# Optimization experiments

Measured on AMD Instinct MI355X. Metric: run time of the kernel, lower is better.

The kernel has to match this reference:

```python
import jax, jax.numpy as jnp
import numpy as np
import math

B, S, E, H = 4, 1024, 768, 12
HD = E // H

def setup_inputs() -> dict:
    key = jax.random.key(0)
    ks = jax.random.split(key, 13)
    inp = {
        'query': jax.random.normal(ks[0], (B, S, E), jnp.float32),
        'key':   jax.random.normal(ks[1], (B, S, E), jnp.float32),
        'value': jax.random.normal(ks[2], (B, S, E), jnp.float32),
        'mask':  jax.random.randint(ks[3], (B, S, S), 0, 2, jnp.int32),
    }
    scale = 1.0 / math.sqrt(E)
    for i, nm in enumerate(['q', 'k', 'v', 'o']):
        inp[f'W{nm}'] = jax.random.normal(ks[4 + 2 * i], (E, E), jnp.float32) * scale
        inp[f'b{nm}'] = jax.random.normal(ks[5 + 2 * i], (E,), jnp.float32) * 0.01
    return inp


def reference(query, key, value, mask, Wq, bq, Wk, bk, Wv, bv, Wo, bo):
    # QKV projections (torch Linear: x @ W.T + b), split into heads -> [B,H,S,HD]
    def proj(x, W, b):
        y = x @ W.T + b
        return y.reshape(B, S, H, HD).transpose(0, 2, 1, 3)

    q = proj(query, Wq, bq)
    k = proj(key, Wk, bk)
    v = proj(value, Wv, bv)

    scores = jnp.einsum('bhqd,bhkd->bhqk', q, k) / jnp.sqrt(jnp.float32(HD))
    m = mask[:, None, :, :]  # [B,1,S,S] broadcast over heads
    # multiply-then-masked_fill semantics of the original module
    scores = scores * m.astype(scores.dtype)
    scores = jnp.where(m == 0, -jnp.inf, scores)
    attn = jax.nn.softmax(scores, axis=-1)
    # nan_to_num for fully-masked rows (all -inf -> NaN -> 0)
    attn = jnp.where(jnp.isnan(attn), 0.0, attn)
    # dropout omitted (eval/deterministic reference)
    xv = jnp.einsum('bhqk,bhkd->bhqd', attn, v)
    xv = xv.transpose(0, 2, 1, 3).reshape(B, S, E)
    out = xv @ Wo.T + bo
    return out
```

## Files before the change

### kernel.cpp

```cpp
#include <hip/hip_runtime.h>

typedef __bf16 bf16x8 __attribute__((ext_vector_type(8)));
typedef float floatx4 __attribute__((ext_vector_type(4)));

#define B_ 4
#define S_ 1024
#define E_ 768
#define H_ 12
#define HD_ 64

__device__ __forceinline__ void async16(const void* g, void* l) {
  __builtin_amdgcn_global_load_lds((const __attribute__((address_space(1))) void*)g,
                                   (__attribute__((address_space(3))) void*)l, 16, 0, 0);
}

__device__ __forceinline__ floatx4 mfma16(bf16x8 a, bf16x8 b, floatx4 c) {
  return __builtin_amdgcn_mfma_f32_16x16x32_bf16(a, b, c, 0, 0, 0);
}

__global__ __launch_bounds__(256) void prep_kernel(
    const float* __restrict__ q, const float* __restrict__ k, const float* __restrict__ v,
    const float* __restrict__ w0, const float* __restrict__ w1,
    const float* __restrict__ w2, const float* __restrict__ w3,
    const int* __restrict__ mask,
    __bf16* __restrict__ xin, __bf16* __restrict__ wb,
    unsigned long long* __restrict__ bm) {
  const int bx = blockIdx.x;
  if (bx < 4608) {
    const int z = bx / 1536, xb = bx % 1536;
    const float* s = (z == 0) ? q : (z == 1) ? k : v;
    __bf16* d = xin + (size_t)z * (size_t)(B_ * S_ * E_);
    const size_t i8 = (size_t)xb * 256 + threadIdx.x;
    const float4* sp = (const float4*)s + i8 * 2;
    float4 a = sp[0], bb = sp[1];
    bf16x8 o;
    o[0] = (__bf16)a.x; o[1] = (__bf16)a.y; o[2] = (__bf16)a.z; o[3] = (__bf16)a.w;
    o[4] = (__bf16)bb.x; o[5] = (__bf16)bb.y; o[6] = (__bf16)bb.z; o[7] = (__bf16)bb.w;
    *(bf16x8*)(d + i8 * 8) = o;
  } else if (bx < 5760) {
    const int t = bx - 4608;
    const int z = t / 288, xb = t % 288;
    const float* s = (z == 0) ? w0 : (z == 1) ? w1 : (z == 2) ? w2 : w3;
    __bf16* d = wb + (size_t)z * (size_t)(E_ * E_);
    const size_t i8 = (size_t)xb * 256 + threadIdx.x;
    const float4* sp = (const float4*)s + i8 * 2;
    float4 a = sp[0], bb = sp[1];
    bf16x8 o;
    o[0] = (__bf16)a.x; o[1] = (__bf16)a.y; o[2] = (__bf16)a.z; o[3] = (__bf16)a.w;
    o[4] = (__bf16)bb.x; o[5] = (__bf16)bb.y; o[6] = (__bf16)bb.z; o[7] = (__bf16)bb.w;
    *(bf16x8*)(d + i8 * 8) = o;
  } else {
    const int row = bx - 5760;
    const int wave = threadIdx.x >> 6, lane = threadIdx.x & 63;
#pragma unroll
    for (int pass = 0; pass < 4; ++pass) {
      const int kk = pass * 256 + wave * 64 + lane;
      const int mv = mask[(size_t)row * S_ + kk];
      const unsigned long long bal = __ballot(mv != 0);
      if (lane == 0) bm[(size_t)row * 16 + pass * 4 + wave] = bal;
    }
  }
}

__global__ __launch_bounds__(256, 2) void proj_qkv_kernel(
    const __bf16* __restrict__ Xq, const __bf16* __restrict__ Xk, const __bf16* __restrict__ Xv,
    const __bf16* __restrict__ Wq, const __bf16* __restrict__ Wk, const __bf16* __restrict__ Wv,
    const float* __restrict__ bq, const float* __restrict__ bk, const float* __restrict__ bv,
    __bf16* __restrict__ Qf, __bf16* __restrict__ Kf, __bf16* __restrict__ Vt) {
  const int z = blockIdx.z;
  const __bf16* X = (z == 0) ? Xq : (z == 1) ? Xk : Xv;
  const __bf16* W = (z == 0) ? Wq : (z == 1) ? Wk : Wv;
  const float* bias = (z == 0) ? bq : (z == 1) ? bk : bv;

  const int tid = threadIdx.x;
  const int wave = tid >> 6, lane = tid & 63;
  const int l15 = lane & 15, quad = lane >> 4;
  const int wr = wave >> 1, wc = wave & 1;
  const int bm = blockIdx.x * 128, bn = blockIdx.y * 128;
  const int srl = lane >> 3, sch = lane & 7;

  __shared__ alignas(16) unsigned char smem[65536];
  __bf16* ST = (__bf16*)smem + (size_t)wave * (64 * 72);

  floatx4 zf = {0.0f, 0.0f, 0.0f, 0.0f};
  floatx4 acc[4][4];
#pragma unroll
  for (int i = 0; i < 4; ++i)
#pragma unroll
    for (int j = 0; j < 4; ++j) acc[i][j] = zf;

#pragma unroll
  for (int c = 0; c < 4; ++c) {
    const int s = c * 4 + wave;
    const int row = s * 8 + srl;
    const int xo = (sch ^ (row & 7)) * 8;
    async16(X + (size_t)(bm + row) * E_ + xo, (__bf16*)smem + s * 512);
    async16(W + (size_t)(bn + row) * E_ + xo, (__bf16*)(smem + 16384) + s * 512);
  }

  for (int kt = 0; kt < 12; ++kt) {
    const int p = kt & 1;
    __bf16* As = (__bf16*)(smem + p * 32768);
    __bf16* Bs = (__bf16*)(smem + p * 32768 + 16384);
    __syncthreads();

    if (kt < 11) {
      const int kk = (kt + 1) * 64;
      __bf16* An = (__bf16*)(smem + (1 - p) * 32768);
      __bf16* Bn = (__bf16*)(smem + (1 - p) * 32768 + 16384);
#pragma unroll
      for (int c = 0; c < 4; ++c) {
        const int s = c * 4 + wave;
        const int row = s * 8 + srl;
        const int xo = (sch ^ (row & 7)) * 8;
        async16(X + (size_t)(bm + row) * E_ + kk + xo, An + s * 512);
        async16(W + (size_t)(bn + row) * E_ + kk + xo, Bn + s * 512);
      }
    }

#pragma unroll
    for (int ks = 0; ks < 2; ++ks) {
      bf16x8 af[4], bfr[4];
#pragma unroll
      for (int i = 0; i < 4; ++i) {
        const int m = wr * 64 + i * 16 + l15;
        af[i] = *(const bf16x8*)&As[m * 64 + (((ks * 4 + quad) ^ (m & 7)) * 8)];
      }
#pragma unroll
      for (int j = 0; j < 4; ++j) {
        const int n = wc * 64 + j * 16 + l15;
        bfr[j] = *(const bf16x8*)&Bs[n * 64 + (((ks * 4 + quad) ^ (n & 7)) * 8)];
      }
#pragma unroll
      for (int i = 0; i < 4; ++i)
#pragma unroll
        for (int j = 0; j < 4; ++j)
          acc[i][j] = mfma16(af[i], bfr[j], acc[i][j]);
    }
  }
  __syncthreads();

  if (z < 2) {
    __bf16* dst = (z == 0) ? Qf : Kf;
    const float sc = (z == 0) ? 0.125f : 1.0f;
#pragma unroll
    for (int j = 0; j < 4; ++j) {
      const float bval = bias[bn + wc * 64 + j * 16 + l15];
#pragma unroll
      for (int i = 0; i < 4; ++i)
#pragma unroll
        for (int r = 0; r < 4; ++r)
          ST[(i * 16 + quad * 4 + r) * 72 + j * 16 + l15] =
              (__bf16)((acc[i][j][r] + bval) * sc);
    }
#pragma unroll
    for (int t = 0; t < 8; ++t) {
      const int row = t * 8 + (lane >> 3), ch = lane & 7;
      bf16x8 vrow = *(const bf16x8*)&ST[row * 72 + ch * 8];
      *(bf16x8*)&dst[(size_t)(bm + wr * 64 + row) * E_ + bn + wc * 64 + ch * 8] = vrow;
    }
  } else {
#pragma unroll
    for (int j = 0; j < 4; ++j) {
      const float bval = bias[bn + wc * 64 + j * 16 + l15];
#pragma unroll
      for (int i = 0; i < 4; ++i)
#pragma unroll
        for (int r = 0; r < 4; ++r)
          ST[(j * 16 + l15) * 72 + i * 16 + quad * 4 + r] = (__bf16)(acc[i][j][r] + bval);
    }
    const int hh = (bn + wc * 64) >> 6;
    const int m0 = bm + wr * 64;
    const int bb = m0 >> 10, ss0 = m0 & 1023;
#pragma unroll
    for (int t = 0; t < 8; ++t) {
      const int d = t * 8 + (lane >> 3), ch = lane & 7;
      bf16x8 vrow = *(const bf16x8*)&ST[d * 72 + ch * 8];
      *(bf16x8*)&Vt[(((size_t)bb * H_ + hh) * HD_ + d) * S_ + ss0 + ch * 8] = vrow;
    }
  }
}

__global__ __launch_bounds__(256, 4) void proj_out_kernel(
    const __bf16* __restrict__ X, const __bf16* __restrict__ W,
    const float* __restrict__ bias, float* __restrict__ out) {
  const int tid = threadIdx.x;
  const int wave = tid >> 6, lane = tid & 63;
  const int l15 = lane & 15, quad = lane >> 4;
  const int wr = wave >> 1, wc = wave & 1;
  const int bm = blockIdx.x * 64, bn = blockIdx.y * 64;
  const int srl = lane >> 3, sch = lane & 7;

  __shared__ alignas(16) unsigned char smem[32768];

  floatx4 zf = {0.0f, 0.0f, 0.0f, 0.0f};
  floatx4 acc[2][2];
#pragma unroll
  for (int i = 0; i < 2; ++i)
#pragma unroll
    for (int j = 0; j < 2; ++j) acc[i][j] = zf;

#pragma unroll
  for (int c = 0; c < 2; ++c) {
    const int s = c * 4 + wave;
    const int row = s * 8 + srl;
    const int xo = (sch ^ (row & 7)) * 8;
    async16(X + (size_t)(bm + row) * E_ + xo, (__bf16*)smem + s * 512);
    async16(W + (size_t)(bn + row) * E_ + xo, (__bf16*)(smem + 8192) + s * 512);
  }

  for (int kt = 0; kt < 12; ++kt) {
    const int p = kt & 1;
    __bf16* As = (__bf16*)(smem + p * 16384);
    __bf16* Bs = (__bf16*)(smem + p * 16384 + 8192);
    __syncthreads();

    if (kt < 11) {
      const int kk = (kt + 1) * 64;
      __bf16* An = (__bf16*)(smem + (1 - p) * 16384);
      __bf16* Bn = (__bf16*)(smem + (1 - p) * 16384 + 8192);
#pragma unroll
      for (int c = 0; c < 2; ++c) {
        const int s = c * 4 + wave;
        const int row = s * 8 + srl;
        const int xo = (sch ^ (row & 7)) * 8;
        async16(X + (size_t)(bm + row) * E_ + kk + xo, An + s * 512);
        async16(W + (size_t)(bn + row) * E_ + kk + xo, Bn + s * 512);
      }
    }

#pragma unroll
    for (int ks = 0; ks < 2; ++ks) {
      bf16x8 af[2], bfr[2];
#pragma unroll
      for (int i = 0; i < 2; ++i) {
        const int m = wr * 32 + i * 16 + l15;
        af[i] = *(const bf16x8*)&As[m * 64 + (((ks * 4 + quad) ^ (m & 7)) * 8)];
      }
#pragma unroll
      for (int j = 0; j < 2; ++j) {
        const int n = wc * 32 + j * 16 + l15;
        bfr[j] = *(const bf16x8*)&Bs[n * 64 + (((ks * 4 + quad) ^ (n & 7)) * 8)];
      }
#pragma unroll
      for (int i = 0; i < 2; ++i)
#pragma unroll
        for (int j = 0; j < 2; ++j)
          acc[i][j] = mfma16(af[i], bfr[j], acc[i][j]);
    }
  }

#pragma unroll
  for (int j = 0; j < 2; ++j) {
    const int n = bn + wc * 32 + j * 16 + l15;
    const float bval = bias[n];
#pragma unroll
    for (int i = 0; i < 2; ++i) {
#pragma unroll
      for (int r = 0; r < 4; ++r) {
        const int m = bm + wr * 32 + i * 16 + quad * 4 + r;
        out[(size_t)m * E_ + n] = acc[i][j][r] + bval;
      }
    }
  }
}

#define MSHIFT 12.0f
#define PSTR 72
__global__ __launch_bounds__(256, 3) void attn_kernel(
    const __bf16* __restrict__ Qf, const __bf16* __restrict__ Kf,
    const __bf16* __restrict__ Vt, const unsigned long long* __restrict__ bmask,
    __bf16* __restrict__ XV) {
  const int tid = threadIdx.x;
  const int wave = tid >> 6, lane = tid & 63;
  const int l15 = lane & 15, quad = lane >> 4;
  const int bh = blockIdx.x;
  const int b = bh / H_, h = bh % H_;
  const int q0 = blockIdx.y * 64 + wave * 16;

  __shared__ alignas(16) __bf16 Kbuf[2][64 * 64];
  __shared__ alignas(16) __bf16 Vbuf[2][64 * 64];
  __shared__ alignas(16) __bf16 Ps[4 * 16 * PSTR];
  __bf16* Pw = &Ps[wave * 16 * PSTR];

  const __bf16* qb = Qf + ((size_t)b * S_ + q0) * E_ + h * HD_;
  bf16x8 af[2];
  af[0] = *(const bf16x8*)(qb + (size_t)l15 * E_ + quad * 8);
  af[1] = *(const bf16x8*)(qb + (size_t)l15 * E_ + 32 + quad * 8);

  const __bf16* kbase = Kf + (size_t)b * S_ * E_ + h * HD_;
  const __bf16* vbase = Vt + (size_t)bh * HD_ * S_;
  const unsigned long long* mbm = bmask + ((size_t)b * S_ + q0) * 16;

  const int srow = tid >> 3, sch = tid & 7;
#pragma unroll
  for (int c = 0; c < 2; ++c) {
    const int row = c * 32 + srow;
    const int xo = (sch ^ (row & 7)) * 8;
    async16(kbase + (size_t)row * E_ + xo, &Kbuf[0][(c * 256 + tid) * 8]);
    async16(vbase + (size_t)row * S_ + xo, &Vbuf[0][(c * 256 + tid) * 8]);
  }

  unsigned long long bmsh[4];
#pragma unroll
  for (int r = 0; r < 4; ++r)
    bmsh[r] = mbm[(size_t)(quad * 4 + r) * 16 + 0] >> l15;

  floatx4 zf = {0.0f, 0.0f, 0.0f, 0.0f};
  floatx4 o[4];
  float lrow[4];
#pragma unroll
  for (int jd = 0; jd < 4; ++jd) o[jd] = zf;
#pragma unroll
  for (int r = 0; r < 4; ++r) lrow[r] = 0.0f;

  for (int kt = 0; kt < 16; ++kt) {
    const int p = kt & 1;
    const int k0 = kt * 64;
    __syncthreads();

    if (kt < 15) {
      const int kn = k0 + 64;
#pragma unroll
      for (int c = 0; c < 2; ++c) {
        const int row = c * 32 + srow;
        const int xo = (sch ^ (row & 7)) * 8;
        async16(kbase + (size_t)(kn + row) * E_ + xo, &Kbuf[1 - p][(c * 256 + tid) * 8]);
        async16(vbase + (size_t)row * S_ + kn + xo, &Vbuf[1 - p][(c * 256 + tid) * 8]);
      }
    }

    unsigned long long bmnext[4];
    if (kt < 15) {
#pragma unroll
      for (int r = 0; r < 4; ++r)
        bmnext[r] = mbm[(size_t)(quad * 4 + r) * 16 + kt + 1] >> l15;
    }

    bf16x8 bk[4][2];
#pragma unroll
    for (int j = 0; j < 4; ++j) {
      const int key = j * 16 + l15;
#pragma unroll
      for (int ks = 0; ks < 2; ++ks)
        bk[j][ks] = *(const bf16x8*)&Kbuf[p][key * 64 + ((ks * 4 + quad) ^ (key & 7)) * 8];
    }
    bf16x8 bvf[4][2];
#pragma unroll
    for (int jd = 0; jd < 4; ++jd) {
      const int d = jd * 16 + l15;
#pragma unroll
      for (int ks2 = 0; ks2 < 2; ++ks2)
        bvf[jd][ks2] = *(const bf16x8*)&Vbuf[p][d * 64 + ((ks2 * 4 + quad) ^ (d & 7)) * 8];
    }

    floatx4 sc[4];
#pragma unroll
    for (int j = 0; j < 4; ++j) sc[j] = zf;
#pragma unroll
    for (int j = 0; j < 4; ++j) {
      sc[j] = mfma16(af[0], bk[j][0], sc[j]);
      sc[j] = mfma16(af[1], bk[j][1], sc[j]);
    }

#pragma unroll
    for (int j = 0; j < 4; ++j)
#pragma unroll
      for (int r = 0; r < 4; ++r) {
        float pv = __expf(sc[j][r] - MSHIFT);
        pv = ((bmsh[r] >> (j * 16)) & 1ull) ? pv : 0.0f;
        lrow[r] += pv;
        Pw[(quad * 4 + r) * PSTR + j * 16 + l15] = (__bf16)pv;
      }

#pragma unroll
    for (int ks2 = 0; ks2 < 2; ++ks2) {
      bf16x8 pa = *(const bf16x8*)&Pw[l15 * PSTR + ks2 * 32 + quad * 8];
#pragma unroll
      for (int jd = 0; jd < 4; ++jd) o[jd] = mfma16(pa, bvf[jd][ks2], o[jd]);
    }

    if (kt < 15) {
#pragma unroll
      for (int r = 0; r < 4; ++r) bmsh[r] = bmnext[r];
    }
  }

#pragma unroll
  for (int sh = 1; sh < 16; sh <<= 1)
#pragma unroll
    for (int r = 0; r < 4; ++r) lrow[r] += __shfl_xor(lrow[r], sh, 64);
  float linv[4];
#pragma unroll
  for (int r = 0; r < 4; ++r) linv[r] = (lrow[r] > 0.0f) ? (1.0f / lrow[r]) : 0.0f;
  __bf16* xbase = XV + ((size_t)b * S_ + q0) * E_ + h * HD_;
#pragma unroll
  for (int jd = 0; jd < 4; ++jd)
#pragma unroll
    for (int r = 0; r < 4; ++r)
      xbase[(size_t)(quad * 4 + r) * E_ + jd * 16 + l15] = (__bf16)(o[jd][r] * linv[r]);
}

extern "C" void kernel_launch(void* const* d_in, const int* in_sizes, int n_in,
                              void* d_out, int out_size, void* d_ws, size_t ws_size,
                              hipStream_t stream) {
  const float* query = (const float*)d_in[0];
  const float* key   = (const float*)d_in[1];
  const float* value = (const float*)d_in[2];
  const int*   mask  = (const int*)d_in[3];
  const float* Wq = (const float*)d_in[4];
  const float* bq = (const float*)d_in[5];
  const float* Wk = (const float*)d_in[6];
  const float* bk = (const float*)d_in[7];
  const float* Wv = (const float*)d_in[8];
  const float* bv = (const float*)d_in[9];
  const float* Wo = (const float*)d_in[10];
  const float* bo = (const float*)d_in[11];
  float* out = (float*)d_out;

  const size_t NX = (size_t)B_ * S_ * E_;
  const size_t NW = (size_t)E_ * E_;
  __bf16* ws = (__bf16*)d_ws;
  __bf16* xq  = ws;
  __bf16* xk  = xq + NX;
  __bf16* xv  = xk + NX;
  __bf16* wqb = xv + NX;
  __bf16* wkb = wqb + NW;
  __bf16* wvb = wkb + NW;
  __bf16* wob = wvb + NW;
  __bf16* Qf  = wob + NW;
  __bf16* Kf  = Qf + NX;
  __bf16* Vt  = Kf + NX;
  __bf16* XVb = Vt + NX;
  unsigned long long* bmask = (unsigned long long*)(XVb + NX);

  prep_kernel<<<dim3(9856), 256, 0, stream>>>(query, key, value, Wq, Wk, Wv, Wo,
                                              mask, xq, wqb, bmask);
  proj_qkv_kernel<<<dim3(32, 6, 3), 256, 0, stream>>>(xq, xk, xv, wqb, wkb, wvb,
                                                      bq, bk, bv, Qf, Kf, Vt);
  attn_kernel<<<dim3(48, 16), 256, 0, stream>>>(Qf, Kf, Vt, bmask, XVb);
  proj_out_kernel<<<dim3(64, 12), 256, 0, stream>>>(XVb, wob, bo, out);
}
```

Before: 183.1 us.

## Fuse fp32-to-bf16 activation conversion into QKV projection A-operand loads

Removes the separate pass that converts the query/key/value fp32 activations to bf16. The QKV projection kernel now reads fp32 activations directly from global memory into registers and converts them to bf16 fragments, with only the weights staged through LDS. This halves LDS use and raises the occupancy hint to 3 blocks per CU. The mask bitpacking also handles 4 rows per block. The cost is direct uncached-pattern global fp32 reads (each row read by both column-waves and across 6 column blocks) without async prefetch, so the A loads may stall the MFMA loop.

```diff
diff --git a/kernel.cpp b/kernel.cpp
--- a/kernel.cpp
+++ b/kernel.cpp
@@ -18,57 +18,50 @@
   return __builtin_amdgcn_mfma_f32_16x16x32_bf16(a, b, c, 0, 0, 0);
 }
 
+__device__ __forceinline__ bf16x8 cvt8(float4 a, float4 b) {
+  bf16x8 o;
+  o[0] = (__bf16)a.x; o[1] = (__bf16)a.y; o[2] = (__bf16)a.z; o[3] = (__bf16)a.w;
+  o[4] = (__bf16)b.x; o[5] = (__bf16)b.y; o[6] = (__bf16)b.z; o[7] = (__bf16)b.w;
+  return o;
+}
+
 __global__ __launch_bounds__(256) void prep_kernel(
-    const float* __restrict__ q, const float* __restrict__ k, const float* __restrict__ v,
     const float* __restrict__ w0, const float* __restrict__ w1,
     const float* __restrict__ w2, const float* __restrict__ w3,
     const int* __restrict__ mask,
-    __bf16* __restrict__ xin, __bf16* __restrict__ wb,
-    unsigned long long* __restrict__ bm) {
+    __bf16* __restrict__ wb, unsigned long long* __restrict__ bm) {
   const int bx = blockIdx.x;
-  if (bx < 4608) {
-    const int z = bx / 1536, xb = bx % 1536;
-    const float* s = (z == 0) ? q : (z == 1) ? k : v;
-    __bf16* d = xin + (size_t)z * (size_t)(B_ * S_ * E_);
-    const size_t i8 = (size_t)xb * 256 + threadIdx.x;
-    const float4* sp = (const float4*)s + i8 * 2;
-    float4 a = sp[0], bb = sp[1];
-    bf16x8 o;
-    o[0] = (__bf16)a.x; o[1] = (__bf16)a.y; o[2] = (__bf16)a.z; o[3] = (__bf16)a.w;
-    o[4] = (__bf16)bb.x; o[5] = (__bf16)bb.y; o[6] = (__bf16)bb.z; o[7] = (__bf16)bb.w;
-    *(bf16x8*)(d + i8 * 8) = o;
-  } else if (bx < 5760) {
-    const int t = bx - 4608;
-    const int z = t / 288, xb = t % 288;
+  if (bx < 1152) {
+    const int z = bx / 288, xb = bx % 288;
     const float* s = (z == 0) ? w0 : (z == 1) ? w1 : (z == 2) ? w2 : w3;
     __bf16* d = wb + (size_t)z * (size_t)(E_ * E_);
     const size_t i8 = (size_t)xb * 256 + threadIdx.x;
     const float4* sp = (const float4*)s + i8 * 2;
-    float4 a = sp[0], bb = sp[1];
-    bf16x8 o;
-    o[0] = (__bf16)a.x; o[1] = (__bf16)a.y; o[2] = (__bf16)a.z; o[3] = (__bf16)a.w;
-    o[4] = (__bf16)bb.x; o[5] = (__bf16)bb.y; o[6] = (__bf16)bb.z; o[7] = (__bf16)bb.w;
-    *(bf16x8*)(d + i8 * 8) = o;
+    *(bf16x8*)(d + i8 * 8) = cvt8(sp[0], sp[1]);
   } else {
-    const int row = bx - 5760;
+    const int row0 = (bx - 1152) * 4;
     const int wave = threadIdx.x >> 6, lane = threadIdx.x & 63;
 #pragma unroll
-    for (int pass = 0; pass < 4; ++pass) {
-      const int kk = pass * 256 + wave * 64 + lane;
-      const int mv = mask[(size_t)row * S_ + kk];
-      const unsigned long long bal = __ballot(mv != 0);
-      if (lane == 0) bm[(size_t)row * 16 + pass * 4 + wave] = bal;
-    }
-  }
-}
-
-__global__ __launch_bounds__(256, 2) void proj_qkv_kernel(
-    const __bf16* __restrict__ Xq, const __bf16* __restrict__ Xk, const __bf16* __restrict__ Xv,
+    for (int rr = 0; rr < 4; ++rr) {
+      const int row = row0 + rr;
+#pragma unroll
+      for (int pass = 0; pass < 4; ++pass) {
+        const int kk = pass * 256 + wave * 64 + lane;
+        const int mv = mask[(size_t)row * S_ + kk];
+        const unsigned long long bal = __ballot(mv != 0);
+        if (lane == 0) bm[(size_t)row * 16 + pass * 4 + wave] = bal;
+      }
+    }
+  }
+}
+
+__global__ __launch_bounds__(256, 3) void proj_qkv_kernel(
+    const float* __restrict__ Xq, const float* __restrict__ Xk, const float* __restrict__ Xv,
     const __bf16* __restrict__ Wq, const __bf16* __restrict__ Wk, const __bf16* __restrict__ Wv,
     const float* __restrict__ bq, const float* __restrict__ bk, const float* __restrict__ bv,
     __bf16* __restrict__ Qf, __bf16* __restrict__ Kf, __bf16* __restrict__ Vt) {
   const int z = blockIdx.z;
-  const __bf16* X = (z == 0) ? Xq : (z == 1) ? Xk : Xv;
+  const float* X = (z == 0) ? Xq : (z == 1) ? Xk : Xv;
   const __bf16* W = (z == 0) ? Wq : (z == 1) ? Wk : Wv;
   const float* bias = (z == 0) ? bq : (z == 1) ? bk : bv;
 
@@ -79,7 +72,7 @@
   const int bm = blockIdx.x * 128, bn = blockIdx.y * 128;
   const int srl = lane >> 3, sch = lane & 7;
 
-  __shared__ alignas(16) unsigned char smem[65536];
+  __shared__ alignas(16) unsigned char smem[36864];
   __bf16* ST = (__bf16*)smem + (size_t)wave * (64 * 72);
 
   floatx4 zf = {0.0f, 0.0f, 0.0f, 0.0f};
@@ -94,38 +87,41 @@
     const int s = c * 4 + wave;
     const int row = s * 8 + srl;
     const int xo = (sch ^ (row & 7)) * 8;
-    async16(X + (size_t)(bm + row) * E_ + xo, (__bf16*)smem + s * 512);
-    async16(W + (size_t)(bn + row) * E_ + xo, (__bf16*)(smem + 16384) + s * 512);
+    async16(W + (size_t)(bn + row) * E_ + xo, (__bf16*)smem + s * 512);
   }
 
   for (int kt = 0; kt < 12; ++kt) {
     const int p = kt & 1;
-    __bf16* As = (__bf16*)(smem + p * 32768);
-    __bf16* Bs = (__bf16*)(smem + p * 32768 + 16384);
+    __bf16* Bs = (__bf16*)(smem + p * 16384);
     __syncthreads();
 
     if (kt < 11) {
       const int kk = (kt + 1) * 64;
-      __bf16* An = (__bf16*)(smem + (1 - p) * 32768);
-      __bf16* Bn = (__bf16*)(smem + (1 - p) * 32768 + 16384);
+      __bf16* Bn = (__bf16*)(smem + (1 - p) * 16384);
 #pragma unroll
       for (int c = 0; c < 4; ++c) {
         const int s = c * 4 + wave;
         const int row = s * 8 + srl;
         const int xo = (sch ^ (row & 7)) * 8;
-        async16(X + (size_t)(bm + row) * E_ + kk + xo, An + s * 512);
         async16(W + (size_t)(bn + row) * E_ + kk + xo, Bn + s * 512);
       }
     }
 
+    bf16x8 af[4][2];
+#pragma unroll
+    for (int i = 0; i < 4; ++i) {
+      const float* xr = X + (size_t)(bm + wr * 64 + i * 16 + l15) * E_ + kt * 64 + quad * 8;
+      float4 p0 = *(const float4*)(xr);
+      float4 p1 = *(const float4*)(xr + 4);
+      float4 p2 = *(const float4*)(xr + 32);
+      float4 p3 = *(const float4*)(xr + 36);
+      af[i][0] = cvt8(p0, p1);
+      af[i][1] = cvt8(p2, p3);
+    }
+
 #pragma unroll
     for (int ks = 0; ks < 2; ++ks) {
-      bf16x8 af[4], bfr[4];
-#pragma unroll
-      for (int i = 0; i < 4; ++i) {
-        const int m = wr * 64 + i * 16 + l15;
-        af[i] = *(const bf16x8*)&As[m * 64 + (((ks * 4 + quad) ^ (m & 7)) * 8)];
-      }
+      bf16x8 bfr[4];
 #pragma unroll
       for (int j = 0; j < 4; ++j) {
         const int n = wc * 64 + j * 16 + l15;
@@ -135,7 +131,7 @@
       for (int i = 0; i < 4; ++i)
 #pragma unroll
         for (int j = 0; j < 4; ++j)
-          acc[i][j] = mfma16(af[i], bfr[j], acc[i][j]);
+          acc[i][j] = mfma16(af[i][ks], bfr[j], acc[i][j]);
     }
   }
   __syncthreads();
@@ -421,10 +417,7 @@
   const size_t NX = (size_t)B_ * S_ * E_;
   const size_t NW = (size_t)E_ * E_;
   __bf16* ws = (__bf16*)d_ws;
-  __bf16* xq  = ws;
-  __bf16* xk  = xq + NX;
-  __bf16* xv  = xk + NX;
-  __bf16* wqb = xv + NX;
+  __bf16* wqb = ws;
   __bf16* wkb = wqb + NW;
   __bf16* wvb = wkb + NW;
   __bf16* wob = wvb + NW;
@@ -434,10 +427,10 @@
   __bf16* XVb = Vt + NX;
   unsigned long long* bmask = (unsigned long long*)(XVb + NX);
 
-  prep_kernel<<<dim3(9856), 256, 0, stream>>>(query, key, value, Wq, Wk, Wv, Wo,
-                                              mask, xq, wqb, bmask);
-  proj_qkv_kernel<<<dim3(32, 6, 3), 256, 0, stream>>>(xq, xk, xv, wqb, wkb, wvb,
-                                                      bq, bk, bv, Qf, Kf, Vt);
+  prep_kernel<<<dim3(2176), 256, 0, stream>>>(Wq, Wk, Wv, Wo, mask, wqb, bmask);
+  proj_qkv_kernel<<<dim3(32, 6, 3), 256, 0, stream>>>(query, key, value,
+                                                      wqb, wkb, wvb, bq, bk, bv,
+                                                      Qf, Kf, Vt);
   attn_kernel<<<dim3(48, 16), 256, 0, stream>>>(Qf, Kf, Vt, bmask, XVb);
   proj_out_kernel<<<dim3(64, 12), 256, 0, stream>>>(XVb, wob, bo, out);
 }
```

Result: slower. 224.1 us (+22.4%).
